# Kernel tuning notes

Hardware: AMD Instinct MI355X
Metric: run time of the kernel (lower is better)

Reference implementation:

```python
import jax, jax.numpy as jnp
import numpy as np

B, H, W = 128, 64, 64
CH = 64            # feature channels (hardcoded self.channels=64)
GH = GW = 8        # glimpse size
HID = 128          # controller_out
NUM_GLIMPSES = 8
BN_EPS = 1e-5


def setup_inputs() -> dict:
    key = jax.random.key(0)
    ks = jax.random.split(key, 16)
    d = {}
    d['image_pairs'] = jax.random.normal(ks[0], (B, 2, H, W), dtype=jnp.float32)
    # ResidualBlock(1 -> 64)
    d['conv1_w'] = jax.random.normal(ks[1], (CH, 1, 3, 3), jnp.float32) * 0.1
    d['conv1_b'] = jnp.zeros((CH,), jnp.float32)
    d['bn1_g'] = jnp.ones((CH,), jnp.float32)
    d['bn1_b'] = jnp.zeros((CH,), jnp.float32)
    d['conv2_w'] = jax.random.normal(ks[2], (CH, CH, 3, 3), jnp.float32) * 0.02
    d['conv2_b'] = jnp.zeros((CH,), jnp.float32)
    d['bn2_g'] = jnp.ones((CH,), jnp.float32)
    d['bn2_b'] = jnp.zeros((CH,), jnp.float32)
    # LSTMCell(input=GH*GW*CH=4096, hidden=128); torch gate order i,f,g,o
    in_sz = GH * GW * CH
    d['w_ih'] = jax.random.normal(ks[3], (4 * HID, in_sz), jnp.float32) * 0.01
    d['w_hh'] = jax.random.normal(ks[4], (4 * HID, HID), jnp.float32) * 0.05
    d['b_ih'] = jnp.zeros((4 * HID,), jnp.float32)
    d['b_hh'] = jnp.zeros((4 * HID,), jnp.float32)
    # glimpser Linear(128 -> 3)
    d['glimpser_w'] = jax.random.normal(ks[5], (3, HID), jnp.float32) * 0.05
    d['glimpser_b'] = jnp.zeros((3,), jnp.float32)
    return d


def _conv3x3(x, w, b):
    # x: (B,C,H,W), w: (O,I,3,3) -> SAME padding, stride 1 (NCHW/OIHW)
    y = jax.lax.conv_general_dilated(x, w, (1, 1), 'SAME',
                                     dimension_numbers=('NCHW', 'OIHW', 'NCHW'))
    return y + b[None, :, None, None]


def _bn(x, g, b):
    # BatchNorm2d in training mode: batch statistics over (N,H,W)
    m = jnp.mean(x, axis=(0, 2, 3), keepdims=True)
    v = jnp.var(x, axis=(0, 2, 3), keepdims=True)
    return (x - m) * jax.lax.rsqrt(v + BN_EPS) * g[None, :, None, None] + b[None, :, None, None]


def _resblock(x, c1w, c1b, g1, b1, c2w, c2b, g2, b2):
    out = jax.nn.relu(_bn(_conv3x3(x, c1w, c1b), g1, b1))
    out = _bn(_conv3x3(out, c2w, c2b), g2, b2)
    # residual add broadcasts (B,1,H,W) -> (B,64,H,W), matching torch
    return jax.nn.relu(out + x)


def _filterbank(delta_caps, center_caps, image_size, glimpse_size):
    # returns (B, glimpse_size, image_size) Cauchy filterbank
    S = float(image_size)
    G = float(glimpse_size)
    centers = (S - 1.0) * (center_caps + 1.0) / 2.0          # (B,)
    deltas = S / G * (1.0 - jnp.abs(delta_caps))             # (B,)
    gammas = jnp.exp(1.0 - 2.0 * jnp.abs(delta_caps))        # (B,)
    gp = jnp.arange(glimpse_size, dtype=jnp.float32) - (G - 1.0) / 2.0
    gp = centers[:, None] + deltas[:, None] * gp[None, :]    # (B, g)
    ip = jnp.arange(image_size, dtype=jnp.float32)           # (S,)
    fx = (ip[None, None, :] - gp[:, :, None]) / gammas[:, None, None]
    fx = 1.0 / (jnp.pi * gammas[:, None, None] * (1.0 + fx * fx))  # (B, g, S)
    fx = fx / (jnp.sum(fx, axis=2, keepdims=True) + 1e-4)
    return fx


def reference(image_pairs, conv1_w, conv1_b, bn1_g, bn1_b,
              conv2_w, conv2_b, bn2_g, bn2_b,
              w_ih, w_hh, b_ih, b_hh, glimpser_w, glimpser_b):
    image_pairs = image_pairs.astype(jnp.float32)
    support = _resblock(image_pairs[:, 0:1], conv1_w, conv1_b, bn1_g, bn1_b,
                        conv2_w, conv2_b, bn2_g, bn2_b)  # (B,64,H,W)
    test = _resblock(image_pairs[:, 1:2], conv1_w, conv1_b, bn1_g, bn1_b,
                     conv2_w, conv2_b, bn2_g, bn2_b)
    bsz = image_pairs.shape[0]
    Hx = jnp.zeros((bsz, HID), jnp.float32)
    Cx = jnp.zeros((bsz, HID), jnp.float32)
    for turn in range(2 * NUM_GLIMPSES):
        imgs = support if (turn % 2) else test
        gp = jnp.tanh(Hx @ glimpser_w.T + glimpser_b)        # (B,3)
        Fh = _filterbank(gp[:, 2], gp[:, 0], imgs.shape[2], GH)  # (B,gh,H)
        Fw = _filterbank(gp[:, 2], gp[:, 1], imgs.shape[3], GW)  # (B,gw,W)
        # glimpse = Fh . image . Fw^T per channel (fused contraction)
        t = jnp.einsum('bgi,bcij->bcgj', Fh, imgs)           # (B,C,gh,W)
        gl = jnp.einsum('bcgj,bwj->bcgw', t, Fw)             # (B,C,gh,gw)
        flat = gl.reshape(bsz, -1)                           # (B, C*gh*gw)
        gates = flat @ w_ih.T + b_ih + Hx @ w_hh.T + b_hh    # (B, 4*HID)
        i, f, g, o = jnp.split(gates, 4, axis=1)
        Cx = jax.nn.sigmoid(f) * Cx + jax.nn.sigmoid(i) * jnp.tanh(g)
        Hx = jax.nn.sigmoid(o) * jnp.tanh(Cx)
    return Hx
```

## Files before the change

kernel.cpp:

```cpp
#include <hip/hip_runtime.h>
#include <math.h>

typedef unsigned short u16;
typedef unsigned int u32;
typedef short bf16x8 __attribute__((ext_vector_type(8)));
typedef float f32x4 __attribute__((ext_vector_type(4)));

#define PI_F 3.14159265358979323846f

__device__ __forceinline__ float bf2f(u16 u){ union{u32 i; float f;} v; v.i=((u32)u)<<16; return v.f; }
__device__ __forceinline__ u16 f2bf(float f){ union{u32 i; float f;} v; v.f=f; u32 r=v.i+0x7fffu+((v.i>>16)&1u); return (u16)(r>>16); }
__device__ __forceinline__ float sigf(float x){ return 1.0f/(1.0f+expf(-x)); }

__global__ __launch_bounds__(256) void wpack_kernel(const float* __restrict__ w2, u16* __restrict__ wpack)
{
  int e = blockIdx.x*256 + threadIdx.x;
  if (e >= 36864) return;
  int k  = e & 31;
  int oc = (e>>5) & 63;
  int tc = e>>11;
  int tap = tc>>1, c = tc&1;
  int ic = c*32 + k;
  wpack[e] = f2bf(w2[(size_t)(oc*64 + ic)*9 + tap]);
}

__global__ __launch_bounds__(256) void conv1_nhwc_kernel(
    const float* __restrict__ imgp, int ch,
    const float* __restrict__ w1, u16* __restrict__ out)
{
  int b = blockIdx.y, tile = blockIdx.x;
  int ty0 = (tile>>2)<<4, tx0 = (tile&3)<<4;
  int tid = threadIdx.x;
  __shared__ float patch[18*18];
  __shared__ float wsm[576];
  const float* ib = imgp + (((size_t)b*2 + ch)<<12);
  for (int e=tid; e<324; e+=256){
    int py = e/18, px = e - py*18;
    int gy = ty0+py-1, gx = tx0+px-1;
    float v = 0.f;
    if (gy>=0 && gy<64 && gx>=0 && gx<64) v = ib[(gy<<6)+gx];
    patch[e] = v;
  }
  for (int e=tid; e<576; e+=256) wsm[e] = w1[e];
  __syncthreads();
  int ty = tid>>4, tx = tid&15;
  float p[9];
  #pragma unroll
  for (int ky=0;ky<3;ky++)
    #pragma unroll
    for (int kx=0;kx<3;kx++) p[ky*3+kx] = patch[(ty+ky)*18 + tx+kx];
  u16* ob = out + ((((size_t)b<<12) + ((size_t)(ty0+ty)<<6) + (size_t)(tx0+tx))<<6);
  #pragma unroll
  for (int ocq=0; ocq<8; ocq++){
    u32 w4[4];
    #pragma unroll
    for (int pair=0; pair<4; pair++){
      float a0=0.f, a1=0.f;
      int oc0 = ocq*8 + pair*2;
      #pragma unroll
      for (int k=0;k<9;k++){ a0 += wsm[oc0*9+k]*p[k]; a1 += wsm[(oc0+1)*9+k]*p[k]; }
      w4[pair] = (u32)f2bf(a0) | ((u32)f2bf(a1)<<16);
    }
    ((uint4*)ob)[ocq] = make_uint4(w4[0],w4[1],w4[2],w4[3]);
  }
}

__device__ __forceinline__ void stats_body(const u16* __restrict__ buf, float* __restrict__ st, int blk, int tid)
{
  int c8 = (tid&7)*8;
  int pg = tid>>3;
  size_t p0 = (size_t)blk*1024 + pg;
  float s[8], s2[8];
  #pragma unroll
  for (int k=0;k<8;k++){ s[k]=0.f; s2[k]=0.f; }
  for (int it=0; it<32; it++){
    size_t p = p0 + (size_t)it*32;
    uint4 v = *(const uint4*)(buf + (p<<6) + c8);
    u32 rw[4] = {v.x,v.y,v.z,v.w};
    #pragma unroll
    for (int d=0; d<4; d++){
      float f0 = bf2f((u16)(rw[d]&0xffff));
      float f1 = bf2f((u16)(rw[d]>>16));
      s[d*2]   += f0; s2[d*2]   += f0*f0;
      s[d*2+1] += f1; s2[d*2+1] += f1*f1;
    }
  }
  #pragma unroll
  for (int off=32; off>=8; off>>=1){
    #pragma unroll
    for (int k=0;k<8;k++){ s[k] += __shfl_down(s[k], off, 64); s2[k] += __shfl_down(s2[k], off, 64); }
  }
  __shared__ float sm[128];
  if (tid<128) sm[tid]=0.f;
  __syncthreads();
  if ((tid&63) < 8){
    int cb = tid&7;
    #pragma unroll
    for (int k=0;k<8;k++){
      atomicAdd(&sm[cb*8+k], s[k]);
      atomicAdd(&sm[64+cb*8+k], s2[k]);
    }
  }
  __syncthreads();
  if (tid<128) atomicAdd(&st[tid], sm[tid]);
}

__global__ __launch_bounds__(256) void stats_nhwc_kernel(const u16* __restrict__ buf, float* __restrict__ st)
{
  stats_body(buf, st, blockIdx.x, threadIdx.x);
}

__global__ __launch_bounds__(256) void stats_pair_kernel(
    const u16* __restrict__ A, const u16* __restrict__ B,
    float* __restrict__ stA, float* __restrict__ stB)
{
  const u16* buf = (blockIdx.x < 512)? A : B;
  float* st = (blockIdx.x < 512)? stA : stB;
  stats_body(buf, st, blockIdx.x & 511, threadIdx.x);
}

__global__ __launch_bounds__(256) void conv2_mfma_kernel(
    const u16* __restrict__ in, const u16* __restrict__ wpack, u16* __restrict__ out,
    const float* __restrict__ st, const float* __restrict__ gam, const float* __restrict__ bet)
{
  int b = blockIdx.y, tile = blockIdx.x;
  int y0 = (tile>>2)*8, x0 = (tile&3)*16;
  int tid = threadIdx.x;
  int w = tid>>6, lane = tid&63;
  int m = lane&15, q = lane>>4;

  __shared__ __align__(16) u16 patch[11520];
  __shared__ float scs[64], shs[64];

  if (tid < 64){
    const float invN = 1.0f/524288.0f;
    float mean = st[tid]*invN;
    float var  = st[64+tid]*invN - mean*mean;
    float sc = gam[tid]*rsqrtf(var+1e-5f);
    scs[tid] = sc;
    shs[tid] = bet[tid] - mean*sc;
  }
  __syncthreads();

  for (int e=tid; e<1440; e+=256){
    int py = e/144; int rem = e - py*144;
    int px = rem>>3, cq = rem&7;
    int y = y0-1+py, x = x0-1+px;
    uint4 v = make_uint4(0,0,0,0);
    if (y>=0 && y<64 && x>=0 && x<64){
      uint4 raw = *(const uint4*)(in + ((((size_t)b<<12) + ((size_t)y<<6) + (size_t)x)<<6) + cq*8);
      u32 rw[4] = {raw.x, raw.y, raw.z, raw.w};
      u32 ow[4];
      #pragma unroll
      for (int d=0; d<4; d++){
        u32 o = 0;
        #pragma unroll
        for (int h=0; h<2; h++){
          int c = cq*8 + d*2 + h;
          float f = bf2f((u16)((rw[d]>>(16*h))&0xffff))*scs[c] + shs[c];
          f = fmaxf(f, 0.f);
          o |= ((u32)f2bf(f)) << (16*h);
        }
        ow[d] = o;
      }
      v = make_uint4(ow[0],ow[1],ow[2],ow[3]);
    }
    *(uint4*)(patch + ((((py<<3)+cq)*18 + px)<<3)) = v;
  }
  __syncthreads();

  f32x4 acc[2][4];
  #pragma unroll
  for (int mt=0;mt<2;mt++)
    #pragma unroll
    for (int nt=0;nt<4;nt++) acc[mt][nt] = (f32x4){0.f,0.f,0.f,0.f};

  #pragma unroll
  for (int tap=0; tap<9; tap++){
    const int dy = tap/3, dx = tap%3;
    #pragma unroll
    for (int c=0; c<2; c++){
      const int kk = tap*2 + c;
      bf16x8 bw[4];
      #pragma unroll
      for (int nt=0; nt<4; nt++)
        bw[nt] = *(const bf16x8*)(wpack + (size_t)(kk*64 + nt*16 + m)*32 + q*8);
      #pragma unroll
      for (int mt=0; mt<2; mt++){
        int py = 2*w + mt + dy;
        bf16x8 av = *(const bf16x8*)(patch + ((((py<<3) + (c<<2) + q)*18 + (m+dx))<<3));
        #pragma unroll
        for (int nt=0; nt<4; nt++)
          acc[mt][nt] = __builtin_amdgcn_mfma_f32_16x16x32_bf16(av, bw[nt], acc[mt][nt], 0,0,0);
      }
    }
  }
  __syncthreads();
  u16* etile = patch;
  #pragma unroll
  for (int mt=0; mt<2; mt++){
    int lp = (2*w+mt)*16 + q*4;
    #pragma unroll
    for (int nt=0; nt<4; nt++)
      #pragma unroll
      for (int r=0; r<4; r++)
        etile[(lp+r)*64 + nt*16 + m] = f2bf(acc[mt][nt][r]);
  }
  __syncthreads();
  int lp = tid>>1, half = tid&1;
  int y = y0 + (lp>>4), x = x0 + (lp&15);
  uint4* gdst = (uint4*)(out + ((((size_t)b<<12) + ((size_t)y<<6) + (size_t)x)<<6) + half*32);
  const uint4* lsrc = (const uint4*)(etile + lp*64 + half*32);
  gdst[0] = lsrc[0];
  gdst[1] = lsrc[1];
  gdst[2] = lsrc[2];
  gdst[3] = lsrc[3];
}

__device__ __forceinline__ void compute_params_lane(
    int b, int lane, float h0, float h1,
    const float* __restrict__ gw, const float* __restrict__ gb,
    float* __restrict__ FhT, float* __restrict__ Fw)
{
  float gpv[3];
  #pragma unroll
  for (int k=0;k<3;k++){
    float p = h0*gw[k*128+lane] + h1*gw[k*128+64+lane];
    #pragma unroll
    for (int off=32; off>0; off>>=1) p += __shfl_down(p, off, 64);
    float tot = __shfl(p, 0, 64);
    gpv[k] = tanhf(tot + gb[k]);
  }
  float ad = fabsf(gpv[2]);
  float delta = 8.0f*(1.0f-ad);
  float gamma = expf(1.0f-2.0f*ad);
  float inv_pg = 1.0f/(PI_F*gamma);
  float fi = (float)lane;
  float ctr = 31.5f*(gpv[0]+1.0f);
  float fh[8];
  #pragma unroll
  for (int g=0; g<8; g++){
    float mu = ctr + delta*((float)g - 3.5f);
    float u = (fi - mu)/gamma;
    float f = inv_pg/(1.0f+u*u);
    float s = f;
    #pragma unroll
    for (int off=32; off>0; off>>=1) s += __shfl_down(s, off, 64);
    s = __shfl(s, 0, 64);
    fh[g] = f/(s + 1e-4f);
  }
  float4* o = (float4*)(FhT + (((size_t)b<<6) + lane)*8);
  o[0] = make_float4(fh[0],fh[1],fh[2],fh[3]);
  o[1] = make_float4(fh[4],fh[5],fh[6],fh[7]);
  ctr = 31.5f*(gpv[1]+1.0f);
  #pragma unroll
  for (int wv=0; wv<8; wv++){
    float mu = ctr + delta*((float)wv - 3.5f);
    float u = (fi - mu)/gamma;
    float f = inv_pg/(1.0f+u*u);
    float s = f;
    #pragma unroll
    for (int off=32; off>0; off>>=1) s += __shfl_down(s, off, 64);
    s = __shfl(s, 0, 64);
    Fw[(((size_t)b<<3)+wv)*64 + lane] = f/(s + 1e-4f);
  }
}

__device__ __forceinline__ void compute_params_lds(
    int lane, int jc, const float* __restrict__ hnew,
    const float* __restrict__ gw, const float* __restrict__ gb,
    float* __restrict__ fh_lds, float* __restrict__ fw_lds)
{
  float h0 = hnew[lane], h1 = hnew[64+lane];
  float gpv[3];
  #pragma unroll
  for (int k=0;k<3;k++){
    float p = h0*gw[k*128+lane] + h1*gw[k*128+64+lane];
    #pragma unroll
    for (int off=32; off>0; off>>=1) p += __shfl_down(p, off, 64);
    float tot = __shfl(p, 0, 64);
    gpv[k] = tanhf(tot + gb[k]);
  }
  float ad = fabsf(gpv[2]);
  float delta = 8.0f*(1.0f-ad);
  float gamma = expf(1.0f-2.0f*ad);
  float inv_pg = 1.0f/(PI_F*gamma);
  float fi = (float)lane;
  float ctr = 31.5f*(gpv[0]+1.0f);
  #pragma unroll
  for (int g=0; g<8; g++){
    float mu = ctr + delta*((float)g - 3.5f);
    float u = (fi - mu)/gamma;
    float f = inv_pg/(1.0f+u*u);
    float s = f;
    #pragma unroll
    for (int off=32; off>0; off>>=1) s += __shfl_down(s, off, 64);
    s = __shfl(s, 0, 64);
    fh_lds[lane*8+g] = f/(s + 1e-4f);
  }
  ctr = 31.5f*(gpv[1]+1.0f);
  #pragma unroll
  for (int wv=0; wv<8; wv++){
    float mu = ctr + delta*((float)wv - 3.5f);
    float u = (fi - mu)/gamma;
    float f = inv_pg/(1.0f+u*u);
    float s = f;
    #pragma unroll
    for (int off=32; off>0; off>>=1) s += __shfl_down(s, off, 64);
    s = __shfl(s, 0, 64);
    int jl = lane - jc*16;
    if (jl >= 0 && jl < 16) fw_lds[jl*8+wv] = f/(s + 1e-4f);
  }
}

__global__ __launch_bounds__(512,4) void glimpse_lstm_kernel(
    const u16* __restrict__ img, const float* __restrict__ part,
    const float* __restrict__ whhT,
    const float* __restrict__ bih, const float* __restrict__ bhh,
    const float* __restrict__ gw, const float* __restrict__ gb,
    const float* __restrict__ Hx_in, const float* __restrict__ Cx_in,
    float* __restrict__ Hx_out, float* __restrict__ Cx_out,
    float* __restrict__ part_gl,
    const float* __restrict__ st2, const float* __restrict__ gam2,
    const float* __restrict__ bet2, const float* __restrict__ imgp,
    int ch, int t)
{
  int jc = blockIdx.x, b = blockIdx.y;
  int tid = threadIdx.x;
  __shared__ float hs[128];
  __shared__ float hnew[128];
  __shared__ float gsm[512];
  __shared__ float scs[64], shs[64];
  __shared__ __align__(16) float fh_lds[512];
  __shared__ __align__(16) float fw_lds[128];
  __shared__ __align__(16) float t_lds[8*16*64];

  if (tid < 64){
    const float invN = 1.0f/524288.0f;
    float mean = st2[tid]*invN;
    float var  = st2[64+tid]*invN - mean*mean;
    float sc = gam2[tid]*rsqrtf(var+1e-5f);
    scs[tid] = sc;
    shs[tid] = bet2[tid] - mean*sc;
  }

  if (t > 0){
    if (tid < 128) hs[tid] = Hx_in[b*128+tid];
    __syncthreads();
    {
      int n = tid;
      float acc = bih[n] + bhh[n];
      const float* pp = part + (size_t)b*16384 + n;
      #pragma unroll 8
      for (int ks=0; ks<32; ks++) acc += pp[ks*512];
      const float* wp = whhT + n;
      #pragma unroll 8
      for (int k=0;k<128;k++) acc += hs[k]*wp[(size_t)k*512];
      gsm[n] = acc;
    }
    __syncthreads();
    if (tid < 128){
      float cx = Cx_in[b*128+tid];
      float cn = sigf(gsm[128+tid])*cx + sigf(gsm[tid])*tanhf(gsm[256+tid]);
      float hn = sigf(gsm[384+tid])*tanhf(cn);
      hnew[tid] = hn;
      if (jc == 0){ Cx_out[b*128+tid] = cn; Hx_out[b*128+tid] = hn; }
    }
  } else {
    if (tid < 128) hnew[tid] = 0.f;
  }
  __syncthreads();

  if (tid < 64) compute_params_lds(tid, jc, hnew, gw, gb, fh_lds, fw_lds);
  __syncthreads();

  int ih = tid>>7, j = (tid>>3)&15, cg = tid&7;
  float scq[8], shq[8];
  #pragma unroll
  for (int k=0;k<8;k++){ scq[k] = scs[cg*8+k]; shq[k] = shs[cg*8+k]; }
  f32x4 accA[8], accB[8];
  #pragma unroll
  for (int g=0;g<8;g++){ accA[g]=(f32x4){0.f,0.f,0.f,0.f}; accB[g]=(f32x4){0.f,0.f,0.f,0.f}; }
  const u16* ib = img + ((((size_t)b<<12) + ((size_t)(ih*16)<<6) + (size_t)(jc*16+j))<<6) + cg*8;
  const float* rp = imgp + (((size_t)(b*2+ch))<<12) + ((size_t)(ih*16)<<6) + (jc*16+j);
  #pragma unroll 8
  for (int ii=0; ii<16; ii++){
    uint4 vv = *(const uint4*)(ib + ((size_t)ii<<12));
    float res = rp[ii<<6];
    float x0=fmaxf(bf2f((u16)(vv.x&0xffff))*scq[0]+shq[0]+res, 0.f);
    float x1=fmaxf(bf2f((u16)(vv.x>>16))   *scq[1]+shq[1]+res, 0.f);
    float x2=fmaxf(bf2f((u16)(vv.y&0xffff))*scq[2]+shq[2]+res, 0.f);
    float x3=fmaxf(bf2f((u16)(vv.y>>16))   *scq[3]+shq[3]+res, 0.f);
    float x4=fmaxf(bf2f((u16)(vv.z&0xffff))*scq[4]+shq[4]+res, 0.f);
    float x5=fmaxf(bf2f((u16)(vv.z>>16))   *scq[5]+shq[5]+res, 0.f);
    float x6=fmaxf(bf2f((u16)(vv.w&0xffff))*scq[6]+shq[6]+res, 0.f);
    float x7=fmaxf(bf2f((u16)(vv.w>>16))   *scq[7]+shq[7]+res, 0.f);
    int i = ih*16+ii;
    f32x4 fa = *(const f32x4*)&fh_lds[i*8];
    f32x4 fb = *(const f32x4*)&fh_lds[i*8+4];
    #pragma unroll
    for (int g=0;g<4;g++){
      accA[g][0]+=fa[g]*x0; accA[g][1]+=fa[g]*x1; accA[g][2]+=fa[g]*x2; accA[g][3]+=fa[g]*x3;
      accB[g][0]+=fa[g]*x4; accB[g][1]+=fa[g]*x5; accB[g][2]+=fa[g]*x6; accB[g][3]+=fa[g]*x7;
      accA[g+4][0]+=fb[g]*x0; accA[g+4][1]+=fb[g]*x1; accA[g+4][2]+=fb[g]*x2; accA[g+4][3]+=fb[g]*x3;
      accB[g+4][0]+=fb[g]*x4; accB[g+4][1]+=fb[g]*x5; accB[g+4][2]+=fb[g]*x6; accB[g+4][3]+=fb[g]*x7;
    }
  }
  if (ih==0){
    #pragma unroll
    for (int g=0;g<8;g++){
      *(f32x4*)&t_lds[(g*16+j)*64 + cg*8]     = accA[g];
      *(f32x4*)&t_lds[(g*16+j)*64 + cg*8 + 4] = accB[g];
    }
  }
  __syncthreads();
  if (ih==1){
    #pragma unroll
    for (int g=0;g<8;g++){
      f32x4* p0 = (f32x4*)&t_lds[(g*16+j)*64 + cg*8];
      p0[0] = p0[0] + accA[g];
      p0[1] = p0[1] + accB[g];
    }
  }
  __syncthreads();
  if (ih==2){
    #pragma unroll
    for (int g=0;g<8;g++){
      f32x4* p0 = (f32x4*)&t_lds[(g*16+j)*64 + cg*8];
      p0[0] = p0[0] + accA[g];
      p0[1] = p0[1] + accB[g];
    }
  }
  __syncthreads();
  if (ih==3){
    #pragma unroll
    for (int g=0;g<8;g++){
      f32x4* p0 = (f32x4*)&t_lds[(g*16+j)*64 + cg*8];
      p0[0] = p0[0] + accA[g];
      p0[1] = p0[1] + accB[g];
    }
  }
  __syncthreads();

  {
    int c = tid&63, s = tid>>6;
    float acc2[8];
    #pragma unroll
    for (int wv=0;wv<8;wv++) acc2[wv]=0.f;
    #pragma unroll
    for (int jl=0; jl<16; jl++){
      float tv = t_lds[(((s<<4)+jl)<<6) + c];
      f32x4 w0 = *(const f32x4*)&fw_lds[jl*8];
      f32x4 w1 = *(const f32x4*)&fw_lds[jl*8+4];
      acc2[0]+=tv*w0[0]; acc2[1]+=tv*w0[1]; acc2[2]+=tv*w0[2]; acc2[3]+=tv*w0[3];
      acc2[4]+=tv*w1[0]; acc2[5]+=tv*w1[1]; acc2[6]+=tv*w1[2]; acc2[7]+=tv*w1[3];
    }
    float* dst = part_gl + (((size_t)(b*4+jc))<<12) + c*64 + s*8;
    *(f32x4*)(dst+0) = (f32x4){acc2[0],acc2[1],acc2[2],acc2[3]};
    *(f32x4*)(dst+4) = (f32x4){acc2[4],acc2[5],acc2[6],acc2[7]};
  }
}

__global__ __launch_bounds__(256) void gemm_ih_kernel(
    const float* __restrict__ part_gl, const float* __restrict__ Bw, float* __restrict__ part)
{
  int n0 = blockIdx.x*32;
  int kb = blockIdx.y;
  int k0 = kb*128;
  __shared__ __align__(16) float Asm[16*132];
  __shared__ __align__(16) float Bsm[16*36];
  int tid = threadIdx.x;
  int tm = tid & 15, tn = tid >> 4;
  float acc[8][2];
  #pragma unroll
  for (int i=0;i<8;i++){ acc[i][0]=0.f; acc[i][1]=0.f; }
  for (int kt=0; kt<128; kt+=16){
    for (int e=tid; e<512; e+=256){
      int mrow = e>>2, kq = e&3;
      const float* pg = part_gl + ((size_t)mrow<<14) + (k0+kt+kq*4);
      float4 a0 = *(const float4*)pg;
      float4 a1 = *(const float4*)(pg+4096);
      float4 a2 = *(const float4*)(pg+8192);
      float4 a3 = *(const float4*)(pg+12288);
      float4 a = make_float4(a0.x+a1.x+a2.x+a3.x, a0.y+a1.y+a2.y+a3.y,
                             a0.z+a1.z+a2.z+a3.z, a0.w+a1.w+a2.w+a3.w);
      Asm[(kq*4+0)*132+mrow] = a.x;
      Asm[(kq*4+1)*132+mrow] = a.y;
      Asm[(kq*4+2)*132+mrow] = a.z;
      Asm[(kq*4+3)*132+mrow] = a.w;
    }
    if (tid < 128){
      int n = tid>>2, kq = tid&3;
      float4 bv = *(const float4*)(Bw + (size_t)(n0+n)*4096 + k0+kt+kq*4);
      Bsm[(kq*4+0)*36+n] = bv.x;
      Bsm[(kq*4+1)*36+n] = bv.y;
      Bsm[(kq*4+2)*36+n] = bv.z;
      Bsm[(kq*4+3)*36+n] = bv.w;
    }
    __syncthreads();
    #pragma unroll
    for (int kk=0;kk<16;kk++){
      float b0 = Bsm[kk*36 + tn*2];
      float b1 = Bsm[kk*36 + tn*2 + 1];
      float4 a0 = *(const float4*)&Asm[kk*132 + tm*8];
      float4 a1 = *(const float4*)&Asm[kk*132 + tm*8 + 4];
      float av[8] = {a0.x,a0.y,a0.z,a0.w,a1.x,a1.y,a1.z,a1.w};
      #pragma unroll
      for (int mm=0;mm<8;mm++){
        acc[mm][0] += av[mm]*b0;
        acc[mm][1] += av[mm]*b1;
      }
    }
    __syncthreads();
  }
  #pragma unroll
  for (int mm=0;mm<8;mm++){
    int mrow = tm*8+mm;
    *(float2*)&part[(size_t)mrow*16384 + kb*512 + n0 + tn*2] =
        make_float2(acc[mm][0],acc[mm][1]);
  }
}

__global__ __launch_bounds__(256) void lstm_update_kernel(
    float* __restrict__ Hx, float* __restrict__ Cx,
    const float* __restrict__ part, const float* __restrict__ whhT,
    const float* __restrict__ b_ih, const float* __restrict__ b_hh,
    const float* __restrict__ gw, const float* __restrict__ gb,
    float* __restrict__ FhT, float* __restrict__ Fw)
{
  int b = blockIdx.x;
  int tid = threadIdx.x;
  int hid = tid & 127, half = tid >> 7;
  __shared__ float hs[128];
  __shared__ float hs2[128];
  __shared__ float gp[1024];
  if (tid < 128) hs[tid] = Hx[b*128+tid];
  __syncthreads();
  #pragma unroll
  for (int qd=0; qd<4; qd++){
    int n = qd*128 + hid;
    float acc = half ? 0.f : (b_ih[n] + b_hh[n]);
    const float* pp = part + (size_t)b*16384 + (size_t)(half*16)*512 + n;
    #pragma unroll
    for (int ks=0; ks<16; ks++) acc += pp[ks*512];
    const float* wp = whhT + n + (size_t)(half*64)*512;
    const float* hp = hs + half*64;
    #pragma unroll 8
    for (int k=0;k<64;k++) acc += hp[k]*wp[(size_t)k*512];
    gp[(half*4+qd)*128 + hid] = acc;
  }
  __syncthreads();
  if (tid < 128){
    float g0 = gp[  0+tid] + gp[512+  0+tid];
    float g1 = gp[128+tid] + gp[512+128+tid];
    float g2 = gp[256+tid] + gp[512+256+tid];
    float g3 = gp[384+tid] + gp[512+384+tid];
    float cx = Cx[b*128+tid];
    float cn = sigf(g1)*cx + sigf(g0)*tanhf(g2);
    float hn = sigf(g3)*tanhf(cn);
    Cx[b*128+tid] = cn;
    Hx[b*128+tid] = hn;
    hs2[tid] = hn;
  }
  __syncthreads();
  if (tid < 64)
    compute_params_lane(b, tid, hs2[tid], hs2[64+tid], gw, gb, FhT, Fw);
}

__global__ __launch_bounds__(256) void transpose_whh_kernel(
    const float* __restrict__ whh, float* __restrict__ whhT)
{
  int idx = blockIdx.x*256 + threadIdx.x;
  int k = idx>>9, n = idx&511;
  whhT[idx] = whh[n*128 + k];
}

extern "C" void kernel_launch(void* const* d_in, const int* in_sizes, int n_in,
                              void* d_out, int out_size, void* d_ws, size_t ws_size,
                              hipStream_t stream)
{
  const float* imgp = (const float*)d_in[0];
  const float* w1  = (const float*)d_in[1];
  const float* g1  = (const float*)d_in[3];
  const float* be1 = (const float*)d_in[4];
  const float* w2  = (const float*)d_in[5];
  const float* g2  = (const float*)d_in[7];
  const float* be2 = (const float*)d_in[8];
  const float* wih = (const float*)d_in[9];
  const float* whh = (const float*)d_in[10];
  const float* bih = (const float*)d_in[11];
  const float* bhh = (const float*)d_in[12];
  const float* gw  = (const float*)d_in[13];
  const float* gb  = (const float*)d_in[14];

  char* ws = (char*)d_ws;
  u16* imgT    = (u16*)(ws + 0);
  u16* imgS    = (u16*)(ws + 67108864);
  u16* tmp     = (u16*)(ws + 134217728);
  float* Hbuf1   = (float*)(ws + 134217728);
  float* cbuf1   = (float*)(ws + 134283264);
  float* part_gl = (float*)(ws + 134742016);
  float* part    = (float*)(ws + 143130624);
  float* whhT    = (float*)(ws + 151519232);
  u16*   wpack   = (u16*)  (ws + 201326592);
  float* Hbuf0   = (float*)(ws + 201400320);
  float* cbuf0   = (float*)(ws + 201465856);
  float* stats   = (float*)(ws + 201531392);
  if (ws_size < 201533440ull) return;

  hipMemsetAsync(Hbuf0, 0, 65536+65536+2048, stream);
  wpack_kernel<<<144,256,0,stream>>>(w2, wpack);

  for (int s=0; s<2; s++){
    int ch = (s==0)?1:0;
    u16* dst = (s==0)? imgT : imgS;
    conv1_nhwc_kernel<<<dim3(16,128),256,0,stream>>>(imgp, ch, w1, tmp);
    stats_nhwc_kernel<<<512,256,0,stream>>>(tmp, stats + 128*(2*s));
    conv2_mfma_kernel<<<dim3(32,128),256,0,stream>>>(tmp, wpack, dst,
        stats + 128*(2*s), g1, be1);
  }
  stats_pair_kernel<<<1024,256,0,stream>>>(imgT, imgS, stats + 128, stats + 384);

  transpose_whh_kernel<<<256,256,0,stream>>>(whh, whhT);

  for (int t=0; t<16; t++){
    int sup = t&1;
    const u16* im = sup? imgS : imgT;
    const float* st2 = sup? (stats+384) : (stats+128);
    int ch = sup? 0 : 1;
    const float* Hin = sup? Hbuf0 : Hbuf1;
    const float* Cin = sup? cbuf0 : cbuf1;
    float* Hout = sup? Hbuf1 : Hbuf0;
    float* Cout = sup? cbuf1 : cbuf0;
    glimpse_lstm_kernel<<<dim3(4,128),512,0,stream>>>(
        im, part, whhT, bih, bhh, gw, gb, Hin, Cin, Hout, Cout, part_gl,
        st2, g2, be2, imgp, ch, t);
    gemm_ih_kernel<<<dim3(16,32),256,0,stream>>>(part_gl, wih, part);
  }
  lstm_update_kernel<<<128,256,0,stream>>>(Hbuf1, cbuf1, part, whhT, bih, bhh, gw, gb,
                                           part_gl, part_gl + 65536 );

  hipMemcpyAsync(d_out, Hbuf1, (size_t)16384*4, hipMemcpyDeviceToDevice, stream);
}
```

Before: 1.427 ms.

## Use bf16 MFMA for input-to-hidden LSTM GEMM with pre-packed bf16 weights

```diff
diff --git a/kernel.cpp b/kernel.cpp
--- a/kernel.cpp
+++ b/kernel.cpp
@@ -22,6 +22,12 @@
   int tap = tc>>1, c = tc&1;
   int ic = c*32 + k;
   wpack[e] = f2bf(w2[(size_t)(oc*64 + ic)*9 + tap]);
+}
+
+__global__ __launch_bounds__(256) void wihpack_kernel(const float* __restrict__ wih, u16* __restrict__ wihb)
+{
+  int e = blockIdx.x*256 + threadIdx.x;
+  wihb[e] = f2bf(wih[e]);
 }
 
 __global__ __launch_bounds__(256) void conv1_nhwc_kernel(
@@ -462,62 +468,73 @@
 }
 
 __global__ __launch_bounds__(256) void gemm_ih_kernel(
-    const float* __restrict__ part_gl, const float* __restrict__ Bw, float* __restrict__ part)
-{
-  int n0 = blockIdx.x*32;
+    const float* __restrict__ part_gl, const u16* __restrict__ wihb, float* __restrict__ part)
+{
+  int n0 = blockIdx.x*128;
   int kb = blockIdx.y;
   int k0 = kb*128;
-  __shared__ __align__(16) float Asm[16*132];
-  __shared__ __align__(16) float Bsm[16*36];
+  __shared__ __align__(16) u16 AsmB[128*32];
+  __shared__ __align__(16) u16 BsmB[128*32];
   int tid = threadIdx.x;
-  int tm = tid & 15, tn = tid >> 4;
-  float acc[8][2];
-  #pragma unroll
-  for (int i=0;i<8;i++){ acc[i][0]=0.f; acc[i][1]=0.f; }
-  for (int kt=0; kt<128; kt+=16){
-    for (int e=tid; e<512; e+=256){
-      int mrow = e>>2, kq = e&3;
-      const float* pg = part_gl + ((size_t)mrow<<14) + (k0+kt+kq*4);
-      float4 a0 = *(const float4*)pg;
-      float4 a1 = *(const float4*)(pg+4096);
-      float4 a2 = *(const float4*)(pg+8192);
-      float4 a3 = *(const float4*)(pg+12288);
-      float4 a = make_float4(a0.x+a1.x+a2.x+a3.x, a0.y+a1.y+a2.y+a3.y,
-                             a0.z+a1.z+a2.z+a3.z, a0.w+a1.w+a2.w+a3.w);
-      Asm[(kq*4+0)*132+mrow] = a.x;
-      Asm[(kq*4+1)*132+mrow] = a.y;
-      Asm[(kq*4+2)*132+mrow] = a.z;
-      Asm[(kq*4+3)*132+mrow] = a.w;
-    }
-    if (tid < 128){
-      int n = tid>>2, kq = tid&3;
-      float4 bv = *(const float4*)(Bw + (size_t)(n0+n)*4096 + k0+kt+kq*4);
-      Bsm[(kq*4+0)*36+n] = bv.x;
-      Bsm[(kq*4+1)*36+n] = bv.y;
-      Bsm[(kq*4+2)*36+n] = bv.z;
-      Bsm[(kq*4+3)*36+n] = bv.w;
+  int w = tid>>6, lane = tid&63;
+  int m = lane&15, q = lane>>4;
+
+  f32x4 acc[2][8];
+  #pragma unroll
+  for (int mf=0;mf<2;mf++)
+    #pragma unroll
+    for (int nf=0;nf<8;nf++) acc[mf][nf] = (f32x4){0.f,0.f,0.f,0.f};
+
+  for (int ks=0; ks<4; ks++){
+    int kbase = k0 + ks*32;
+    {
+      int mr = tid & 127, half = tid >> 7;
+      const float* pg = part_gl + ((size_t)mr<<14) + kbase + half*16;
+      u16 tmpv[16];
+      #pragma unroll
+      for (int kq=0; kq<4; kq++){
+        float4 a0 = *(const float4*)(pg + kq*4);
+        float4 a1 = *(const float4*)(pg + 4096 + kq*4);
+        float4 a2 = *(const float4*)(pg + 8192 + kq*4);
+        float4 a3 = *(const float4*)(pg + 12288 + kq*4);
+        tmpv[kq*4+0] = f2bf(a0.x+a1.x+a2.x+a3.x);
+        tmpv[kq*4+1] = f2bf(a0.y+a1.y+a2.y+a3.y);
+        tmpv[kq*4+2] = f2bf(a0.z+a1.z+a2.z+a3.z);
+        tmpv[kq*4+3] = f2bf(a0.w+a1.w+a2.w+a3.w);
+      }
+      *(uint4*)(AsmB + mr*32 + half*16)     = *(uint4*)&tmpv[0];
+      *(uint4*)(AsmB + mr*32 + half*16 + 8) = *(uint4*)&tmpv[8];
+    }
+    {
+      int n = tid & 127, half = tid >> 7;
+      const u16* wp = wihb + (size_t)(n0+n)*4096 + kbase + half*16;
+      uint4 b0 = *(const uint4*)wp;
+      uint4 b1 = *(const uint4*)(wp+8);
+      *(uint4*)(BsmB + n*32 + half*16)     = b0;
+      *(uint4*)(BsmB + n*32 + half*16 + 8) = b1;
     }
     __syncthreads();
     #pragma unroll
-    for (int kk=0;kk<16;kk++){
-      float b0 = Bsm[kk*36 + tn*2];
-      float b1 = Bsm[kk*36 + tn*2 + 1];
-      float4 a0 = *(const float4*)&Asm[kk*132 + tm*8];
-      float4 a1 = *(const float4*)&Asm[kk*132 + tm*8 + 4];
-      float av[8] = {a0.x,a0.y,a0.z,a0.w,a1.x,a1.y,a1.z,a1.w};
-      #pragma unroll
-      for (int mm=0;mm<8;mm++){
-        acc[mm][0] += av[mm]*b0;
-        acc[mm][1] += av[mm]*b1;
+    for (int mf=0; mf<2; mf++){
+      bf16x8 av = *(const bf16x8*)(AsmB + ((w*2+mf)*16 + m)*32 + q*8);
+      #pragma unroll
+      for (int nf=0; nf<8; nf++){
+        bf16x8 bw = *(const bf16x8*)(BsmB + (nf*16 + m)*32 + q*8);
+        acc[mf][nf] = __builtin_amdgcn_mfma_f32_16x16x32_bf16(av, bw, acc[mf][nf], 0,0,0);
       }
     }
     __syncthreads();
   }
   #pragma unroll
-  for (int mm=0;mm<8;mm++){
-    int mrow = tm*8+mm;
-    *(float2*)&part[(size_t)mrow*16384 + kb*512 + n0 + tn*2] =
-        make_float2(acc[mm][0],acc[mm][1]);
+  for (int mf=0; mf<2; mf++){
+    #pragma unroll
+    for (int r=0; r<4; r++){
+      int mrow = (w*2+mf)*16 + q*4 + r;
+      float* pp = part + (size_t)mrow*16384 + kb*512 + n0;
+      #pragma unroll
+      for (int nf=0; nf<8; nf++)
+        pp[nf*16 + m] = acc[mf][nf][r];
+    }
   }
 }
 
@@ -602,6 +619,7 @@
   float* part_gl = (float*)(ws + 134742016);
   float* part    = (float*)(ws + 143130624);
   float* whhT    = (float*)(ws + 151519232);
+  u16*   wihb    = (u16*)  (ws + 151781376);
   u16*   wpack   = (u16*)  (ws + 201326592);
   float* Hbuf0   = (float*)(ws + 201400320);
   float* cbuf0   = (float*)(ws + 201465856);
@@ -622,6 +640,7 @@
   stats_pair_kernel<<<1024,256,0,stream>>>(imgT, imgS, stats + 128, stats + 384);
 
   transpose_whh_kernel<<<256,256,0,stream>>>(whh, whhT);
+  wihpack_kernel<<<8192,256,0,stream>>>(wih, wihb);
 
   for (int t=0; t<16; t++){
     int sup = t&1;
@@ -635,7 +654,7 @@
     glimpse_lstm_kernel<<<dim3(4,128),512,0,stream>>>(
         im, part, whhT, bih, bhh, gw, gb, Hin, Cin, Hout, Cout, part_gl,
         st2, g2, be2, imgp, ch, t);
-    gemm_ih_kernel<<<dim3(16,32),256,0,stream>>>(part_gl, wih, part);
+    gemm_ih_kernel<<<dim3(4,32),256,0,stream>>>(part_gl, wihb, part);
   }
   lstm_update_kernel<<<128,256,0,stream>>>(Hbuf1, cbuf1, part, whhT, bih, bhh, gw, gb,
                                            part_gl, part_gl + 65536 );
```

Measured after the change: 1.297 ms. -9.1%, faster.
